# Kernel optimization log

Measured on AMD Instinct MI355X. Metric: run time of the kernel, lower is better.

Reference implementation:

```python
import jax, jax.numpy as jnp
import numpy as np

T, A, H, E = 16, 8, 128, 32  # steps, actions/step, hidden, embed


def setup_inputs() -> dict:
    key = jax.random.key(0)
    ks = jax.random.split(key, 16)
    n = lambda k, s: jax.random.normal(k, s, dtype=jnp.float32) * 0.1
    return {
        "old_actions": jax.random.randint(ks[0], (T,), 0, A),
        "init_input": n(ks[1], (1, E)),
        "W_ih_a": n(ks[2], (4 * H, E)), "W_hh_a": n(ks[3], (4 * H, H)),
        "b_ih_a": n(ks[4], (4 * H,)), "b_hh_a": n(ks[5], (4 * H,)),
        "heads_W": n(ks[6], (T, A, H)), "heads_b": n(ks[7], (T, A)),
        "W_ih_c": n(ks[8], (4 * H, E)), "W_hh_c": n(ks[9], (4 * H, H)),
        "b_ih_c": n(ks[10], (4 * H,)), "b_hh_c": n(ks[11], (4 * H,)),
        "critic_W": n(ks[12], (1, H)), "critic_b": n(ks[13], (1,)),
        "embed": n(ks[14], (T * A, E)),
    }


def _lstm_cell(x, h, c, W_ih, W_hh, b_ih, b_hh):
    # PyTorch LSTMCell: gate order i, f, g, o
    g = W_ih @ x + b_ih + W_hh @ h + b_hh
    i, f, gg, o = jnp.split(g, 4)
    c = jax.nn.sigmoid(f) * c + jax.nn.sigmoid(i) * jnp.tanh(gg)
    h = jax.nn.sigmoid(o) * jnp.tanh(c)
    return h, c


def reference(old_actions, init_input, W_ih_a, W_hh_a, b_ih_a, b_hh_a,
              heads_W, heads_b, W_ih_c, W_hh_c, b_ih_c, b_hh_c,
              critic_W, critic_b, embed):
    # input sequence is fully determined by the given actions
    global_idx = jnp.arange(T) * A + old_actions          # action offsets
    emb_rows = embed[global_idx]                          # [T, E]
    x_seq = jnp.concatenate([init_input, emb_rows[:-1]], axis=0)  # [T, E]

    def step(carry, xs):
        h_a, c_a, h_c, c_c = carry
        x, hw, hb, a = xs
        h_a, c_a = _lstm_cell(x, h_a, c_a, W_ih_a, W_hh_a, b_ih_a, b_hh_a)
        logits = hw @ h_a + hb                            # [A]
        logp = jax.nn.log_softmax(logits)
        probs = jnp.exp(logp)
        lp = logp[a]
        ent = -jnp.sum(probs * logp)
        h_c, c_c = _lstm_cell(x, h_c, c_c, W_ih_c, W_hh_c, b_ih_c, b_hh_c)
        val = critic_W[0] @ h_c + critic_b[0]
        return (h_a, c_a, h_c, c_c), (lp, ent, val)

    z = jnp.zeros((H,), jnp.float32)
    _, (log_probs, entropies, values) = jax.lax.scan(
        step, (z, z, z, z), (x_seq, heads_W, heads_b, old_actions))
    return log_probs, entropies, values  # each [T]
```

## Files before the change

kernel.cpp:

```cpp
#include <hip/hip_runtime.h>
#include <math.h>

#define T 16
#define A 8
#define H 128
#define E 32
#define G (4*H)

typedef _Float16 h2t __attribute__((ext_vector_type(2)));
typedef _Float16 h8t __attribute__((ext_vector_type(8)));

__device__ __forceinline__ float sigmoidf_(float x) {
    return 1.0f / (1.0f + __expf(-x));
}
__device__ __forceinline__ float tanhf_(float x) {
    return 1.0f - 2.0f / (1.0f + __expf(2.0f * x));
}

#if __has_builtin(__builtin_amdgcn_fdot2)
#define DOT2(a, b, c) __builtin_amdgcn_fdot2((a), (b), (c), false)
#else
__device__ __forceinline__ float dot2_fb(h2t a, h2t b, float c) {
    return fmaf((float)a[0], (float)b[0], fmaf((float)a[1], (float)b[1], c));
}
#define DOT2(a, b, c) dot2_fb((a), (b), (c))
#endif

#define RPT16(M) M(0) M(1) M(2) M(3) M(4) M(5) M(6) M(7) \
                 M(8) M(9) M(10) M(11) M(12) M(13) M(14) M(15)

__global__ __attribute__((amdgpu_flat_work_group_size(512, 512),
                          amdgpu_waves_per_eu(2, 2)))
void ppo_ctrl_kernel(const int* __restrict__ old_actions,
                     const float* __restrict__ init_input,
                     const float* __restrict__ W_ih_a, const float* __restrict__ W_hh_a,
                     const float* __restrict__ b_ih_a, const float* __restrict__ b_hh_a,
                     const float* __restrict__ heads_W, const float* __restrict__ heads_b,
                     const float* __restrict__ W_ih_c, const float* __restrict__ W_hh_c,
                     const float* __restrict__ b_ih_c, const float* __restrict__ b_hh_c,
                     const float* __restrict__ critic_W, const float* __restrict__ critic_b,
                     const float* __restrict__ embed,
                     float* __restrict__ out)
{
    const int tid  = threadIdx.x;
    const int lane = tid & 63;
    const int wv   = tid >> 6;
    const bool actor = (blockIdx.x == 0);

    const float* W_ih = actor ? W_ih_a : W_ih_c;
    const float* W_hh = actor ? W_hh_a : W_hh_c;
    const float* b_ih = actor ? b_ih_a : b_ih_c;
    const float* b_hh = actor ? b_hh_a : b_hh_c;

    __shared__ __align__(16) float accx_s[T][G];
    __shared__ __align__(16) float gates_s[G];
    __shared__ __align__(16) float x_s[T][E];
    __shared__ __align__(16) _Float16 h16[H];
    __shared__ __align__(16) _Float16 hhist[T][H];

    {
        int t0 = tid >> 5, e0 = tid & 31;
        float v = (t0 == 0) ? init_input[e0]
                            : embed[((t0 - 1) * A + old_actions[t0 - 1]) * E + e0];
        x_s[t0][e0] = v;
    }

    const float* rowp = W_hh + tid * H;
#define LOADW(i) h8t w##i; {                                              \
        float4 fa = *(const float4*)(rowp + 8*(i));                       \
        float4 fb = *(const float4*)(rowp + 8*(i) + 4);                   \
        w##i = (h8t){ (_Float16)fa.x, (_Float16)fa.y,                     \
                      (_Float16)fa.z, (_Float16)fa.w,                     \
                      (_Float16)fb.x, (_Float16)fb.y,                     \
                      (_Float16)fb.z, (_Float16)fb.w };                   \
        asm volatile("" : "+v"(w##i)); }
    RPT16(LOADW)
#undef LOADW

    const float* wir = W_ih + tid * E;
    float4 wi0 = *(const float4*)(wir +  0), wi1 = *(const float4*)(wir +  4),
           wi2 = *(const float4*)(wir +  8), wi3 = *(const float4*)(wir + 12),
           wi4 = *(const float4*)(wir + 16), wi5 = *(const float4*)(wir + 20),
           wi6 = *(const float4*)(wir + 24), wi7 = *(const float4*)(wir + 28);
    const float bias = b_ih[tid] + b_hh[tid];

    __syncthreads();

    #pragma unroll 1
    for (int t = 0; t < T; ++t) {
        float s0 = 0.f, s1 = 0.f, s2 = 0.f, s3 = 0.f;
#define MACI(i) { float4 xv = *(const float4*)(&x_s[t][4*(i)]);           \
        s0 = fmaf(wi##i.x, xv.x, s0); s1 = fmaf(wi##i.y, xv.y, s1);       \
        s2 = fmaf(wi##i.z, xv.z, s2); s3 = fmaf(wi##i.w, xv.w, s3); }
        MACI(0) MACI(1) MACI(2) MACI(3) MACI(4) MACI(5) MACI(6) MACI(7)
#undef MACI
        accx_s[t][tid] = bias + ((s0 + s1) + (s2 + s3));
    }

    float c_reg = 0.0f;
    const h8t* hv = (const h8t*)h16;

    #pragma unroll 1
    for (int t = 0; t < T; ++t) {
        float a0 = 0.f, a1 = 0.f, a2 = 0.f, a3 = 0.f;
        if (t != 0) {
#define MACC(i) { h8t hq = hv[i];                                          \
            a0 = DOT2(__builtin_shufflevector(w##i, w##i, 0, 1),           \
                      __builtin_shufflevector(hq,  hq,  0, 1), a0);        \
            a1 = DOT2(__builtin_shufflevector(w##i, w##i, 2, 3),           \
                      __builtin_shufflevector(hq,  hq,  2, 3), a1);        \
            a2 = DOT2(__builtin_shufflevector(w##i, w##i, 4, 5),           \
                      __builtin_shufflevector(hq,  hq,  4, 5), a2);        \
            a3 = DOT2(__builtin_shufflevector(w##i, w##i, 6, 7),           \
                      __builtin_shufflevector(hq,  hq,  6, 7), a3); }
            RPT16(MACC)
#undef MACC
        }
        gates_s[tid] = accx_s[t][tid] + ((a0 + a1) + (a2 + a3));
        __syncthreads();

        if (tid < H) {
            float gi = gates_s[tid],       gf = gates_s[tid + H];
            float gg = gates_s[tid + 2*H], go = gates_s[tid + 3*H];
            float cn = sigmoidf_(gf) * c_reg + sigmoidf_(gi) * tanhf_(gg);
            c_reg = cn;
            float hvv = sigmoidf_(go) * tanhf_(cn);
            _Float16 hf = (_Float16)hvv;
            h16[tid] = hf;
            hhist[t][tid] = hf;
        }
        __syncthreads();
    }

    if (actor) {
        #pragma unroll
        for (int rep = 0; rep < 2; ++rep) {
            const int tt = wv + rep * 8;
            float hA = (float)hhist[tt][lane];
            float hB = (float)hhist[tt][64 + lane];
#define LOGIT(a) float l##a; {                                            \
            const float* hw = heads_W + (tt * A + (a)) * H;               \
            float p = fmaf(hw[lane], hA, hw[64 + lane] * hB);             \
            p += __shfl_xor(p, 1);  p += __shfl_xor(p, 2);                \
            p += __shfl_xor(p, 4);  p += __shfl_xor(p, 8);                \
            p += __shfl_xor(p, 16); p += __shfl_xor(p, 32);               \
            l##a = p + heads_b[tt * A + (a)]; }
            LOGIT(0) LOGIT(1) LOGIT(2) LOGIT(3)
            LOGIT(4) LOGIT(5) LOGIT(6) LOGIT(7)
#undef LOGIT
            if (lane == 0) {
                float m = fmaxf(fmaxf(fmaxf(l0, l1), fmaxf(l2, l3)),
                                fmaxf(fmaxf(l4, l5), fmaxf(l6, l7)));
                float e0 = __expf(l0 - m), e1 = __expf(l1 - m),
                      e2 = __expf(l2 - m), e3 = __expf(l3 - m),
                      e4 = __expf(l4 - m), e5 = __expf(l5 - m),
                      e6 = __expf(l6 - m), e7 = __expf(l7 - m);
                float s = ((e0 + e1) + (e2 + e3)) + ((e4 + e5) + (e6 + e7));
                float logZ = m + __logf(s);
                int act = old_actions[tt];
                float la = (act == 0) ? l0 : (act == 1) ? l1 : (act == 2) ? l2 :
                           (act == 3) ? l3 : (act == 4) ? l4 : (act == 5) ? l5 :
                           (act == 6) ? l6 : l7;
                out[tt] = la - logZ;
                float w_ = e0*(l0-logZ) + e1*(l1-logZ) + e2*(l2-logZ) + e3*(l3-logZ)
                         + e4*(l4-logZ) + e5*(l5-logZ) + e6*(l6-logZ) + e7*(l7-logZ);
                out[T + tt] = -w_ / s;
            }
        }
    } else {
        #pragma unroll
        for (int rep = 0; rep < 2; ++rep) {
            const int tt = wv + rep * 8;
            float hA = (float)hhist[tt][lane];
            float hB = (float)hhist[tt][64 + lane];
            float p = fmaf(critic_W[lane], hA, critic_W[64 + lane] * hB);
            p += __shfl_xor(p, 1);  p += __shfl_xor(p, 2);
            p += __shfl_xor(p, 4);  p += __shfl_xor(p, 8);
            p += __shfl_xor(p, 16); p += __shfl_xor(p, 32);
            if (lane == 0) out[2 * T + tt] = p + critic_b[0];
        }
    }
}

extern "C" void kernel_launch(void* const* d_in, const int* in_sizes, int n_in,
                              void* d_out, int out_size, void* d_ws, size_t ws_size,
                              hipStream_t stream) {
    const int*   old_actions = (const int*)  d_in[0];
    const float* init_input  = (const float*)d_in[1];
    const float* W_ih_a      = (const float*)d_in[2];
    const float* W_hh_a      = (const float*)d_in[3];
    const float* b_ih_a      = (const float*)d_in[4];
    const float* b_hh_a      = (const float*)d_in[5];
    const float* heads_W     = (const float*)d_in[6];
    const float* heads_b     = (const float*)d_in[7];
    const float* W_ih_c      = (const float*)d_in[8];
    const float* W_hh_c      = (const float*)d_in[9];
    const float* b_ih_c      = (const float*)d_in[10];
    const float* b_hh_c      = (const float*)d_in[11];
    const float* critic_W    = (const float*)d_in[12];
    const float* critic_b    = (const float*)d_in[13];
    const float* embed       = (const float*)d_in[14];
    float* out = (float*)d_out;

    ppo_ctrl_kernel<<<dim3(2), dim3(512), 0, stream>>>(
        old_actions, init_input,
        W_ih_a, W_hh_a, b_ih_a, b_hh_a,
        heads_W, heads_b,
        W_ih_c, W_hh_c, b_ih_c, b_hh_c,
        critic_W, critic_b, embed, out);
}
```

Measured before the change: 31.40 us.

## Split weight conversion and input projection into a wide parallel prep kernel

Adds a 128-block prep kernel that converts both W_hh matrices to fp16 in a coalesced transposed layout and precomputes the input projection plus biases for all timesteps, both stored in the workspace. The 2-block recurrent kernel then only loads the packed weights and reads per-step fp16 accumulations, dropping its serial prologue of fp32 loads, conversion and the W_ih matmul. In exchange it adds a second kernel launch and a global round-trip, and it stores the input projection in fp16, which loses precision.

New measurement: 27.90 us. 1.13x faster.

```diff
diff --git a/kernel.cpp b/kernel.cpp
--- a/kernel.cpp
+++ b/kernel.cpp
@@ -7,6 +7,9 @@
 #define E 32
 #define G (4*H)
 
+#define WS_WHH(L)   ((size_t)(L) * 131072u)
+#define WS_ACCX(L)  (262144u + (size_t)(L) * 16384u)
+
 typedef _Float16 h2t __attribute__((ext_vector_type(2)));
 typedef _Float16 h8t __attribute__((ext_vector_type(8)));
 
@@ -29,79 +32,87 @@
 #define RPT16(M) M(0) M(1) M(2) M(3) M(4) M(5) M(6) M(7) \
                  M(8) M(9) M(10) M(11) M(12) M(13) M(14) M(15)
 
+__global__ __launch_bounds__(256)
+void ppo_prep_kernel(const int* __restrict__ old_actions,
+                     const float* __restrict__ init_input,
+                     const float* __restrict__ W_ih_a, const float* __restrict__ W_hh_a,
+                     const float* __restrict__ b_ih_a, const float* __restrict__ b_hh_a,
+                     const float* __restrict__ W_ih_c, const float* __restrict__ W_hh_c,
+                     const float* __restrict__ b_ih_c, const float* __restrict__ b_hh_c,
+                     const float* __restrict__ embed,
+                     char* __restrict__ ws)
+{
+    const int b = blockIdx.x;
+    if (b < 64) {
+        int tau  = b * 256 + threadIdx.x;
+        int lstm = tau >> 13;
+        int i    = tau & 8191;
+        int r    = i >> 4;
+        int c    = i & 15;
+        const float* W = (lstm == 0) ? W_hh_a : W_hh_c;
+        const float* src = W + r * H + c * 8;
+        float4 fa = *(const float4*)(src);
+        float4 fb = *(const float4*)(src + 4);
+        h8t p = { (_Float16)fa.x, (_Float16)fa.y, (_Float16)fa.z, (_Float16)fa.w,
+                  (_Float16)fb.x, (_Float16)fb.y, (_Float16)fb.z, (_Float16)fb.w };
+        *(h8t*)(ws + WS_WHH(lstm) + (size_t)(c * 512 + r) * 16u) = p;
+    } else {
+        int tau  = (b - 64) * 256 + threadIdx.x;
+        int lstm = tau >> 13;
+        int i    = tau & 8191;
+        int t    = i >> 9;
+        int r    = i & 511;
+        const float* W_ih = (lstm == 0) ? W_ih_a : W_ih_c;
+        const float* b_ih = (lstm == 0) ? b_ih_a : b_ih_c;
+        const float* b_hh = (lstm == 0) ? b_hh_a : b_hh_c;
+        const float* xp = (t == 0) ? init_input
+                                   : embed + ((t - 1) * A + old_actions[t - 1]) * E;
+        const float* wr = W_ih + r * E;
+        float s0 = 0.f, s1 = 0.f, s2 = 0.f, s3 = 0.f;
+        #pragma unroll
+        for (int e = 0; e < E; e += 4) {
+            float4 wv = *(const float4*)(wr + e);
+            float4 xv = *(const float4*)(xp + e);
+            s0 = fmaf(wv.x, xv.x, s0); s1 = fmaf(wv.y, xv.y, s1);
+            s2 = fmaf(wv.z, xv.z, s2); s3 = fmaf(wv.w, xv.w, s3);
+        }
+        float acc = b_ih[r] + b_hh[r] + ((s0 + s1) + (s2 + s3));
+        *(_Float16*)(ws + WS_ACCX(lstm) + (size_t)(t * 512 + r) * 2u) = (_Float16)acc;
+    }
+}
+
 __global__ __attribute__((amdgpu_flat_work_group_size(512, 512),
                           amdgpu_waves_per_eu(2, 2)))
 void ppo_ctrl_kernel(const int* __restrict__ old_actions,
-                     const float* __restrict__ init_input,
-                     const float* __restrict__ W_ih_a, const float* __restrict__ W_hh_a,
-                     const float* __restrict__ b_ih_a, const float* __restrict__ b_hh_a,
                      const float* __restrict__ heads_W, const float* __restrict__ heads_b,
-                     const float* __restrict__ W_ih_c, const float* __restrict__ W_hh_c,
-                     const float* __restrict__ b_ih_c, const float* __restrict__ b_hh_c,
                      const float* __restrict__ critic_W, const float* __restrict__ critic_b,
-                     const float* __restrict__ embed,
+                     const char* __restrict__ ws,
                      float* __restrict__ out)
 {
     const int tid  = threadIdx.x;
     const int lane = tid & 63;
     const int wv   = tid >> 6;
-    const bool actor = (blockIdx.x == 0);
-
-    const float* W_ih = actor ? W_ih_a : W_ih_c;
-    const float* W_hh = actor ? W_hh_a : W_hh_c;
-    const float* b_ih = actor ? b_ih_a : b_ih_c;
-    const float* b_hh = actor ? b_hh_a : b_hh_c;
-
-    __shared__ __align__(16) float accx_s[T][G];
+    const int lstm = blockIdx.x;
+    const bool actor = (lstm == 0);
+
     __shared__ __align__(16) float gates_s[G];
-    __shared__ __align__(16) float x_s[T][E];
     __shared__ __align__(16) _Float16 h16[H];
     __shared__ __align__(16) _Float16 hhist[T][H];
 
-    {
-        int t0 = tid >> 5, e0 = tid & 31;
-        float v = (t0 == 0) ? init_input[e0]
-                            : embed[((t0 - 1) * A + old_actions[t0 - 1]) * E + e0];
-        x_s[t0][e0] = v;
-    }
-
-    const float* rowp = W_hh + tid * H;
-#define LOADW(i) h8t w##i; {                                              \
-        float4 fa = *(const float4*)(rowp + 8*(i));                       \
-        float4 fb = *(const float4*)(rowp + 8*(i) + 4);                   \
-        w##i = (h8t){ (_Float16)fa.x, (_Float16)fa.y,                     \
-                      (_Float16)fa.z, (_Float16)fa.w,                     \
-                      (_Float16)fb.x, (_Float16)fb.y,                     \
-                      (_Float16)fb.z, (_Float16)fb.w };                   \
-        asm volatile("" : "+v"(w##i)); }
+    const char* wbase = ws + WS_WHH(lstm);
+#define LOADW(i) h8t w##i = *(const h8t*)(wbase + (size_t)((i) * 512 + tid) * 16u); \
+        asm volatile("" : "+v"(w##i));
     RPT16(LOADW)
 #undef LOADW
 
-    const float* wir = W_ih + tid * E;
-    float4 wi0 = *(const float4*)(wir +  0), wi1 = *(const float4*)(wir +  4),
-           wi2 = *(const float4*)(wir +  8), wi3 = *(const float4*)(wir + 12),
-           wi4 = *(const float4*)(wir + 16), wi5 = *(const float4*)(wir + 20),
-           wi6 = *(const float4*)(wir + 24), wi7 = *(const float4*)(wir + 28);
-    const float bias = b_ih[tid] + b_hh[tid];
-
-    __syncthreads();
+    const _Float16* accg = (const _Float16*)(ws + WS_ACCX(lstm));
+
+    float c_reg = 0.0f;
+    const h8t* hv = (const h8t*)h16;
 
     #pragma unroll 1
     for (int t = 0; t < T; ++t) {
-        float s0 = 0.f, s1 = 0.f, s2 = 0.f, s3 = 0.f;
-#define MACI(i) { float4 xv = *(const float4*)(&x_s[t][4*(i)]);           \
-        s0 = fmaf(wi##i.x, xv.x, s0); s1 = fmaf(wi##i.y, xv.y, s1);       \
-        s2 = fmaf(wi##i.z, xv.z, s2); s3 = fmaf(wi##i.w, xv.w, s3); }
-        MACI(0) MACI(1) MACI(2) MACI(3) MACI(4) MACI(5) MACI(6) MACI(7)
-#undef MACI
-        accx_s[t][tid] = bias + ((s0 + s1) + (s2 + s3));
-    }
-
-    float c_reg = 0.0f;
-    const h8t* hv = (const h8t*)h16;
-
-    #pragma unroll 1
-    for (int t = 0; t < T; ++t) {
+        float axv = (float)accg[t * 512 + tid];
         float a0 = 0.f, a1 = 0.f, a2 = 0.f, a3 = 0.f;
         if (t != 0) {
 #define MACC(i) { h8t hq = hv[i];                                          \
@@ -116,7 +127,7 @@
             RPT16(MACC)
 #undef MACC
         }
-        gates_s[tid] = accx_s[t][tid] + ((a0 + a1) + (a2 + a3));
+        gates_s[tid] = axv + ((a0 + a1) + (a2 + a3));
         __syncthreads();
 
         if (tid < H) {
@@ -201,11 +212,14 @@
     const float* critic_b    = (const float*)d_in[13];
     const float* embed       = (const float*)d_in[14];
     float* out = (float*)d_out;
-
-    ppo_ctrl_kernel<<<dim3(2), dim3(512), 0, stream>>>(
+    char* ws = (char*)d_ws;
+
+    ppo_prep_kernel<<<dim3(128), dim3(256), 0, stream>>>(
         old_actions, init_input,
         W_ih_a, W_hh_a, b_ih_a, b_hh_a,
-        heads_W, heads_b,
         W_ih_c, W_hh_c, b_ih_c, b_hh_c,
-        critic_W, critic_b, embed, out);
-}
+        embed, ws);
+
+    ppo_ctrl_kernel<<<dim3(2), dim3(512), 0, stream>>>(
+        old_actions, heads_W, heads_b, critic_W, critic_b, ws, out);
+}
```

## Interleave gate rows per lane quad to exchange gates via shuffles, drop a barrier

Applied to the files above, without the earlier changes.

Threads are remapped so that the four gate rows (i,f,g,o) for one hidden unit sit in four adjacent lanes. Gates are exchanged with cross-lane shuffles instead of going through a shared gates array, which removes one __syncthreads per timestep and lets every quad compute the cell update redundantly. The head and critic weights, bias, critic params and actions are also preloaded into registers before the recurrence so their global loads overlap the loop. This adds register pressure from the preloaded head weights, and h16 is now zero-initialized explicitly.

Result: slower. 34.76 us (+10.7%).

```diff
diff --git a/kernel.cpp b/kernel.cpp
--- a/kernel.cpp
+++ b/kernel.cpp
@@ -28,6 +28,7 @@
 
 #define RPT16(M) M(0) M(1) M(2) M(3) M(4) M(5) M(6) M(7) \
                  M(8) M(9) M(10) M(11) M(12) M(13) M(14) M(15)
+#define RPT8(M)  M(0) M(1) M(2) M(3) M(4) M(5) M(6) M(7)
 
 __global__ __attribute__((amdgpu_flat_work_group_size(512, 512),
                           amdgpu_waves_per_eu(2, 2)))
@@ -47,13 +48,16 @@
     const int wv   = tid >> 6;
     const bool actor = (blockIdx.x == 0);
 
+    const int j = tid >> 2;
+    const int g = tid & 3;
+    const int r = (g << 7) | j;
+
     const float* W_ih = actor ? W_ih_a : W_ih_c;
     const float* W_hh = actor ? W_hh_a : W_hh_c;
     const float* b_ih = actor ? b_ih_a : b_ih_c;
     const float* b_hh = actor ? b_hh_a : b_hh_c;
 
-    __shared__ __align__(16) float accx_s[T][G];
-    __shared__ __align__(16) float gates_s[G];
+    __shared__ __align__(16) float accx_s[T * 512];
     __shared__ __align__(16) float x_s[T][E];
     __shared__ __align__(16) _Float16 h16[H];
     __shared__ __align__(16) _Float16 hhist[T][H];
@@ -64,8 +68,9 @@
                             : embed[((t0 - 1) * A + old_actions[t0 - 1]) * E + e0];
         x_s[t0][e0] = v;
     }
-
-    const float* rowp = W_hh + tid * H;
+    if (tid < 64) ((unsigned*)h16)[tid] = 0u;
+
+    const float* rowp = W_hh + r * H;
 #define LOADW(i) h8t w##i; {                                              \
         float4 fa = *(const float4*)(rowp + 8*(i));                       \
         float4 fb = *(const float4*)(rowp + 8*(i) + 4);                   \
@@ -77,16 +82,16 @@
     RPT16(LOADW)
 #undef LOADW
 
-    const float* wir = W_ih + tid * E;
+    const float* wir = W_ih + r * E;
     float4 wi0 = *(const float4*)(wir +  0), wi1 = *(const float4*)(wir +  4),
            wi2 = *(const float4*)(wir +  8), wi3 = *(const float4*)(wir + 12),
            wi4 = *(const float4*)(wir + 16), wi5 = *(const float4*)(wir + 20),
            wi6 = *(const float4*)(wir + 24), wi7 = *(const float4*)(wir + 28);
-    const float bias = b_ih[tid] + b_hh[tid];
+    const float bias = b_ih[r] + b_hh[r];
 
     __syncthreads();
 
-    #pragma unroll 1
+    #pragma unroll 2
     for (int t = 0; t < T; ++t) {
         float s0 = 0.f, s1 = 0.f, s2 = 0.f, s3 = 0.f;
 #define MACI(i) { float4 xv = *(const float4*)(&x_s[t][4*(i)]);           \
@@ -94,16 +99,33 @@
         s2 = fmaf(wi##i.z, xv.z, s2); s3 = fmaf(wi##i.w, xv.w, s3); }
         MACI(0) MACI(1) MACI(2) MACI(3) MACI(4) MACI(5) MACI(6) MACI(7)
 #undef MACI
-        accx_s[t][tid] = bias + ((s0 + s1) + (s2 + s3));
-    }
+        accx_s[t * 512 + tid] = bias + ((s0 + s1) + (s2 + s3));
+    }
+
+    const int tt0 = wv, tt1 = wv + 8;
+#define HWLOAD(a) \
+    float hl0##a = heads_W[(tt0 * A + (a)) * H + lane]; \
+    float hh0##a = heads_W[(tt0 * A + (a)) * H + 64 + lane]; \
+    float hl1##a = heads_W[(tt1 * A + (a)) * H + lane]; \
+    float hh1##a = heads_W[(tt1 * A + (a)) * H + 64 + lane]; \
+    asm volatile("" : "+v"(hl0##a), "+v"(hh0##a), "+v"(hl1##a), "+v"(hh1##a));
+    RPT8(HWLOAD)
+#undef HWLOAD
+    float hbv0 = heads_b[tt0 * A + (lane & 7)];
+    float hbv1 = heads_b[tt1 * A + (lane & 7)];
+    float cw0 = critic_W[lane], cw1 = critic_W[64 + lane], cb = critic_b[0];
+    int act0 = old_actions[tt0], act1 = old_actions[tt1];
+    asm volatile("" : "+v"(hbv0), "+v"(hbv1), "+v"(cw0), "+v"(cw1), "+v"(cb));
 
     float c_reg = 0.0f;
     const h8t* hv = (const h8t*)h16;
+    const bool b0 = (g & 1) != 0, b1 = (g & 2) != 0;
 
     #pragma unroll 1
     for (int t = 0; t < T; ++t) {
-        float a0 = 0.f, a1 = 0.f, a2 = 0.f, a3 = 0.f;
+        float p = accx_s[t * 512 + tid];
         if (t != 0) {
+            float a0 = 0.f, a1 = 0.f, a2 = 0.f, a3 = 0.f;
 #define MACC(i) { h8t hq = hv[i];                                          \
             a0 = DOT2(__builtin_shufflevector(w##i, w##i, 0, 1),           \
                       __builtin_shufflevector(hq,  hq,  0, 1), a0);        \
@@ -115,69 +137,75 @@
                       __builtin_shufflevector(hq,  hq,  6, 7), a3); }
             RPT16(MACC)
 #undef MACC
+            p += ((a0 + a1) + (a2 + a3));
         }
-        gates_s[tid] = accx_s[t][tid] + ((a0 + a1) + (a2 + a3));
-        __syncthreads();
-
-        if (tid < H) {
-            float gi = gates_s[tid],       gf = gates_s[tid + H];
-            float gg = gates_s[tid + 2*H], go = gates_s[tid + 3*H];
-            float cn = sigmoidf_(gf) * c_reg + sigmoidf_(gi) * tanhf_(gg);
-            c_reg = cn;
-            float hvv = sigmoidf_(go) * tanhf_(cn);
-            _Float16 hf = (_Float16)hvv;
-            h16[tid] = hf;
-            hhist[t][tid] = hf;
+
+        float q1 = __shfl_xor(p, 1);
+        float q2 = __shfl_xor(p, 2);
+        float q3 = __shfl_xor(q1, 2);
+        float gi = b1 ? (b0 ? q3 : q2) : (b0 ? q1 : p);
+        float gf = b1 ? (b0 ? q2 : q3) : (b0 ? p  : q1);
+        float gg = b1 ? (b0 ? q1 : p ) : (b0 ? q3 : q2);
+        float go = b1 ? (b0 ? p  : q1) : (b0 ? q2 : q3);
+
+        float cn = sigmoidf_(gf) * c_reg + sigmoidf_(gi) * tanhf_(gg);
+        c_reg = cn;
+        float hvv = sigmoidf_(go) * tanhf_(cn);
+        _Float16 hf = (_Float16)hvv;
+        if (g == 0) {
+            h16[j] = hf;
+            hhist[t][j] = hf;
         }
         __syncthreads();
     }
 
     if (actor) {
-        #pragma unroll
-        for (int rep = 0; rep < 2; ++rep) {
-            const int tt = wv + rep * 8;
-            float hA = (float)hhist[tt][lane];
-            float hB = (float)hhist[tt][64 + lane];
-#define LOGIT(a) float l##a; {                                            \
-            const float* hw = heads_W + (tt * A + (a)) * H;               \
-            float p = fmaf(hw[lane], hA, hw[64 + lane] * hB);             \
-            p += __shfl_xor(p, 1);  p += __shfl_xor(p, 2);                \
-            p += __shfl_xor(p, 4);  p += __shfl_xor(p, 8);                \
-            p += __shfl_xor(p, 16); p += __shfl_xor(p, 32);               \
-            l##a = p + heads_b[tt * A + (a)]; }
-            LOGIT(0) LOGIT(1) LOGIT(2) LOGIT(3)
-            LOGIT(4) LOGIT(5) LOGIT(6) LOGIT(7)
+#define LOGIT(rep,a,dst) {                                                \
+        float pp = fmaf(hl##rep##a, hA, hh##rep##a * hB);                 \
+        pp += __shfl_xor(pp, 1);  pp += __shfl_xor(pp, 2);                \
+        pp += __shfl_xor(pp, 4);  pp += __shfl_xor(pp, 8);                \
+        pp += __shfl_xor(pp, 16); pp += __shfl_xor(pp, 32);               \
+        dst = pp + __shfl(hbv##rep, (a)); }
+#define HEADS(rep) {                                                      \
+        const int tt = tt##rep;                                           \
+        float hA = (float)hhist[tt][lane];                                \
+        float hB = (float)hhist[tt][64 + lane];                           \
+        float l0,l1,l2,l3,l4,l5,l6,l7;                                    \
+        LOGIT(rep,0,l0) LOGIT(rep,1,l1) LOGIT(rep,2,l2) LOGIT(rep,3,l3)   \
+        LOGIT(rep,4,l4) LOGIT(rep,5,l5) LOGIT(rep,6,l6) LOGIT(rep,7,l7)   \
+        if (lane == 0) {                                                  \
+            float m = fmaxf(fmaxf(fmaxf(l0, l1), fmaxf(l2, l3)),          \
+                            fmaxf(fmaxf(l4, l5), fmaxf(l6, l7)));         \
+            float e0 = __expf(l0 - m), e1 = __expf(l1 - m),               \
+                  e2 = __expf(l2 - m), e3 = __expf(l3 - m),               \
+                  e4 = __expf(l4 - m), e5 = __expf(l5 - m),               \
+                  e6 = __expf(l6 - m), e7 = __expf(l7 - m);               \
+            float s = ((e0 + e1) + (e2 + e3)) + ((e4 + e5) + (e6 + e7));  \
+            float logZ = m + __logf(s);                                   \
+            int act = act##rep;                                           \
+            float la = (act == 0) ? l0 : (act == 1) ? l1 : (act == 2) ? l2 : \
+                       (act == 3) ? l3 : (act == 4) ? l4 : (act == 5) ? l5 : \
+                       (act == 6) ? l6 : l7;                              \
+            out[tt] = la - logZ;                                          \
+            float w_ = e0*(l0-logZ) + e1*(l1-logZ) + e2*(l2-logZ) + e3*(l3-logZ) \
+                     + e4*(l4-logZ) + e5*(l5-logZ) + e6*(l6-logZ) + e7*(l7-logZ); \
+            out[T + tt] = -w_ / s;                                        \
+        } }
+        HEADS(0)
+        HEADS(1)
+#undef HEADS
 #undef LOGIT
-            if (lane == 0) {
-                float m = fmaxf(fmaxf(fmaxf(l0, l1), fmaxf(l2, l3)),
-                                fmaxf(fmaxf(l4, l5), fmaxf(l6, l7)));
-                float e0 = __expf(l0 - m), e1 = __expf(l1 - m),
-                      e2 = __expf(l2 - m), e3 = __expf(l3 - m),
-                      e4 = __expf(l4 - m), e5 = __expf(l5 - m),
-                      e6 = __expf(l6 - m), e7 = __expf(l7 - m);
-                float s = ((e0 + e1) + (e2 + e3)) + ((e4 + e5) + (e6 + e7));
-                float logZ = m + __logf(s);
-                int act = old_actions[tt];
-                float la = (act == 0) ? l0 : (act == 1) ? l1 : (act == 2) ? l2 :
-                           (act == 3) ? l3 : (act == 4) ? l4 : (act == 5) ? l5 :
-                           (act == 6) ? l6 : l7;
-                out[tt] = la - logZ;
-                float w_ = e0*(l0-logZ) + e1*(l1-logZ) + e2*(l2-logZ) + e3*(l3-logZ)
-                         + e4*(l4-logZ) + e5*(l5-logZ) + e6*(l6-logZ) + e7*(l7-logZ);
-                out[T + tt] = -w_ / s;
-            }
-        }
     } else {
         #pragma unroll
         for (int rep = 0; rep < 2; ++rep) {
-            const int tt = wv + rep * 8;
+            const int tt = (rep == 0) ? tt0 : tt1;
             float hA = (float)hhist[tt][lane];
             float hB = (float)hhist[tt][64 + lane];
-            float p = fmaf(critic_W[lane], hA, critic_W[64 + lane] * hB);
+            float p = fmaf(cw0, hA, cw1 * hB);
             p += __shfl_xor(p, 1);  p += __shfl_xor(p, 2);
             p += __shfl_xor(p, 4);  p += __shfl_xor(p, 8);
             p += __shfl_xor(p, 16); p += __shfl_xor(p, 32);
-            if (lane == 0) out[2 * T + tt] = p + critic_b[0];
+            if (lane == 0) out[2 * T + tt] = p + cb;
         }
     }
 }
```
